# Kernel tuning notes

Measured on AMD Instinct MI355X. Metric: run time of the kernel, lower is better.

## Reference

```python
import jax, jax.numpy as jnp
import numpy as np

EPS = 1e-6

def _l2normalize(x, axis=1):
    # matches torch: x / sqrt(sum(x^2) + eps)
    norm = jnp.sqrt(jnp.sum(x * x, axis=axis, keepdims=True) + EPS)
    return x / norm


def setup_inputs() -> dict:
    key = jax.random.key(0)
    k1, k2, k3 = jax.random.split(key, 3)
    B, C, H, W = 8, 64, 48, 48
    x = jax.random.normal(k1, (B, C, H, W), dtype=jnp.float32)
    v = jax.random.normal(k2, (B, C, H, W), dtype=jnp.float32)
    pos = jax.random.normal(k3, (B, C, H, W), dtype=jnp.float32)
    # learned scalar parameters (init values from the torch module)
    gamma = jnp.float32(0.0)
    beta_gamma = jnp.float32(10.0)
    sum_gamma0 = jnp.float32(0.0)
    sum_gamma1 = jnp.float32(0.0)
    return {"x": x, "v": v, "pos": pos, "gamma": gamma,
            "beta_gamma": beta_gamma, "sum_gamma0": sum_gamma0,
            "sum_gamma1": sum_gamma1}


def reference(x, v, pos, gamma, beta_gamma, sum_gamma0, sum_gamma1):
    B, C, H, W = x.shape
    N = H * W
    # q and k are computed identically in the original module; compute once.
    q = _l2normalize(x + gamma * pos, axis=1)          # [B, C, H, W]
    qf = q.reshape(B, C, N)                             # [B, C, N]
    vf = v.reshape(B, v.shape[1], N)                    # [B, Cv, N]
    # scores[b, n, m] = <q[:, n], k[:, m]>; learned temperature beta_gamma
    scores = jnp.einsum('bcn,bcm->bnm', qf, qf) * beta_gamma  # [B, N, N]
    beta = jax.nn.softmax(scores, axis=-1)              # [B, N, N]
    # o = v @ beta^T  => o[b, c, n] = sum_m v[b, c, m] * beta[b, n, m]
    o = jnp.einsum('bcm,bnm->bcn', vf, beta).reshape(B, vf.shape[1], H, W)
    e0 = jnp.exp(sum_gamma0)
    e1 = jnp.exp(sum_gamma1)
    tot = e0 + e1
    out = (e0 / tot) * o + (e1 / tot) * v
    return out, beta.reshape(B, N, H, W)
```

## Files before the change

kernel.cpp:

```cpp
#include <hip/hip_runtime.h>
#include <hip/hip_bf16.h>

#define B_  8
#define C_  64
#define N_  2304
#define TS  64
#define NT_ (N_ / TS)
#define LDP 72

typedef __attribute__((ext_vector_type(8))) short  short8;
typedef __attribute__((ext_vector_type(4))) float  floatx4;

struct Hdr { int f32mode; float gamma, bg, cmax, w0, w1; };

__device__ __forceinline__ float bf2f(unsigned short u) {
  return __uint_as_float(((unsigned int)u) << 16);
}
__device__ __forceinline__ unsigned short f2bf(float f) {
  unsigned int x = __float_as_uint(f);
  x += 0x7fff + ((x >> 16) & 1);
  return (unsigned short)(x >> 16);
}

__global__ void detect_k(const void* g, const void* bgp, const void* s0,
                         const void* s1, Hdr* h) {
  if (threadIdx.x == 0 && blockIdx.x == 0) {
    int f32 = (((const unsigned short*)bgp)[0] == 0) ? 1 : 0;
    float gamma, bg, sg0, sg1;
    if (f32) {
      gamma = ((const float*)g)[0];  bg  = ((const float*)bgp)[0];
      sg0   = ((const float*)s0)[0]; sg1 = ((const float*)s1)[0];
    } else {
      gamma = bf2f(((const unsigned short*)g)[0]);
      bg    = bf2f(((const unsigned short*)bgp)[0]);
      sg0   = bf2f(((const unsigned short*)s0)[0]);
      sg1   = bf2f(((const unsigned short*)s1)[0]);
    }
    float e0 = __expf(sg0), e1 = __expf(sg1);
    h->f32mode = f32;
    h->gamma = gamma;
    h->bg = bg;
    h->cmax = fabsf(bg);
    h->w0 = e0 / (e0 + e1);
    h->w1 = e1 / (e0 + e1);
  }
}

__global__ __launch_bounds__(256)
void prep_q(const void* __restrict__ xv, const void* __restrict__ posv,
            const void* __restrict__ vv_raw, const Hdr* __restrict__ h,
            unsigned short* __restrict__ qT, unsigned short* __restrict__ vb) {
  int t = blockIdx.x * 256 + threadIdx.x;
  int b = t / N_;
  int n = t - b * N_;
  const bool f32 = h->f32mode;
  float gamma = h->gamma;
  float vals[C_];
  float s = 0.f;
  if (f32) {
    const float* xp = (const float*)xv  + (size_t)b * C_ * N_ + n;
    const float* pp = (const float*)posv + (size_t)b * C_ * N_ + n;
#pragma unroll
    for (int c = 0; c < C_; ++c) {
      float val = xp[(size_t)c * N_] + gamma * pp[(size_t)c * N_];
      vals[c] = val;  s += val * val;
    }
  } else {
    const unsigned short* xp = (const unsigned short*)xv  + (size_t)b * C_ * N_ + n;
    const unsigned short* pp = (const unsigned short*)posv + (size_t)b * C_ * N_ + n;
#pragma unroll
    for (int c = 0; c < C_; ++c) {
      float val = bf2f(xp[(size_t)c * N_]) + gamma * bf2f(pp[(size_t)c * N_]);
      vals[c] = val;  s += val * val;
    }
  }
  float inv = rsqrtf(s + 1e-6f);
  unsigned int* qrow = reinterpret_cast<unsigned int*>(qT + (size_t)t * C_);
#pragma unroll
  for (int c = 0; c < C_; c += 2) {
    qrow[c >> 1] = (unsigned int)f2bf(vals[c] * inv)
                 | ((unsigned int)f2bf(vals[c + 1] * inv) << 16);
  }
  const int NU32 = (B_ * C_ * N_) / 2;
  const int TC   = (B_ * N_);
  unsigned int* vb32 = reinterpret_cast<unsigned int*>(vb);
  if (f32) {
    const float* vf = (const float*)vv_raw;
    for (int i = t; i < NU32; i += TC) {
      float f0 = vf[2 * i], f1 = vf[2 * i + 1];
      vb32[i] = (unsigned int)f2bf(f0) | ((unsigned int)f2bf(f1) << 16);
    }
  } else {
    const unsigned int* v32 = (const unsigned int*)vv_raw;
    for (int i = t; i < NU32; i += TC) vb32[i] = v32[i];
  }
}

__global__ __launch_bounds__(256)
void pass1_rowsum(const unsigned short* __restrict__ qT,
                  const Hdr* __restrict__ h,
                  float* __restrict__ rowsum) {
  __shared__ unsigned short qm[TS * LDP];
  int b  = blockIdx.x / NT_;
  int n0 = (blockIdx.x - b * NT_) * TS;
  int tid  = threadIdx.x;
  int wave = tid >> 6;
  int lane = tid & 63;
  int quad = lane >> 4;
  int l15  = lane & 15;
  float bg = h->bg, cmax = h->cmax;
  const unsigned short* abase =
      qT + ((size_t)(b * N_ + n0 + 16 * wave + l15)) * C_ + quad * 8;
  short8 a0 = *reinterpret_cast<const short8*>(abase);
  short8 a1 = *reinterpret_cast<const short8*>(abase + 32);
  float acc[4] = {0.f, 0.f, 0.f, 0.f};
  for (int mt = 0; mt < NT_; ++mt) {
    int m0 = mt * TS;
    __syncthreads();
#pragma unroll
    for (int k = 0; k < 2; ++k) {
      int chunk = tid + 256 * k;
      int row = chunk >> 3;
      int col = (chunk & 7) * 8;
      short8 vv = *reinterpret_cast<const short8*>(
          qT + ((size_t)(b * N_ + m0 + row)) * C_ + col);
      *reinterpret_cast<short8*>(&qm[row * LDP + col]) = vv;
    }
    __syncthreads();
#pragma unroll
    for (int j = 0; j < 4; ++j) {
      short8 b0 = *reinterpret_cast<const short8*>(&qm[(j * 16 + l15) * LDP + quad * 8]);
      short8 b1 = *reinterpret_cast<const short8*>(&qm[(j * 16 + l15) * LDP + 32 + quad * 8]);
      floatx4 d = {0.f, 0.f, 0.f, 0.f};
      d = __builtin_amdgcn_mfma_f32_16x16x32_bf16(a0, b0, d, 0, 0, 0);
      d = __builtin_amdgcn_mfma_f32_16x16x32_bf16(a1, b1, d, 0, 0, 0);
#pragma unroll
      for (int r = 0; r < 4; ++r)
        acc[r] += __expf(d[r] * bg - cmax);
    }
  }
#pragma unroll
  for (int r = 0; r < 4; ++r) {
    float vv = acc[r];
    vv += __shfl_xor(vv, 1);
    vv += __shfl_xor(vv, 2);
    vv += __shfl_xor(vv, 4);
    vv += __shfl_xor(vv, 8);
    acc[r] = vv;
  }
  if (l15 == 0) {
#pragma unroll
    for (int r = 0; r < 4; ++r)
      rowsum[(size_t)b * N_ + n0 + 16 * wave + quad * 4 + r] = acc[r];
  }
}

__global__ __launch_bounds__(256)
void pass2_attn(const unsigned short* __restrict__ qT,
                const unsigned short* __restrict__ vb,
                const void* __restrict__ vraw,
                const Hdr* __restrict__ h,
                const float* __restrict__ rowsum,
                void* __restrict__ dout) {
  __shared__ unsigned short qm[TS * LDP];
  __shared__ unsigned short vt[TS * LDP];
  __shared__ unsigned short pt[TS * LDP];
  int b  = blockIdx.x / NT_;
  int n0 = (blockIdx.x - b * NT_) * TS;
  int tid  = threadIdx.x;
  int wave = tid >> 6;
  int lane = tid & 63;
  int quad = lane >> 4;
  int l15  = lane & 15;
  const bool f32 = h->f32mode;
  float bg = h->bg, cmax = h->cmax, w0 = h->w0, w1 = h->w1;
  unsigned short* out16  = (unsigned short*)dout;
  unsigned short* beta16 = out16 + (size_t)B_ * C_ * N_;
  float* out32  = (float*)dout;
  float* beta32 = out32 + (size_t)B_ * C_ * N_;

  const unsigned short* abase =
      qT + ((size_t)(b * N_ + n0 + 16 * wave + l15)) * C_ + quad * 8;
  short8 a0 = *reinterpret_cast<const short8*>(abase);
  short8 a1 = *reinterpret_cast<const short8*>(abase + 32);
  float inv[4];
#pragma unroll
  for (int r = 0; r < 4; ++r)
    inv[r] = 1.f / rowsum[(size_t)b * N_ + n0 + 16 * wave + quad * 4 + r];
  floatx4 oacc[4] = {{0.f,0.f,0.f,0.f},{0.f,0.f,0.f,0.f},
                     {0.f,0.f,0.f,0.f},{0.f,0.f,0.f,0.f}};
  for (int mt = 0; mt < NT_; ++mt) {
    int m0 = mt * TS;
    __syncthreads();
#pragma unroll
    for (int k = 0; k < 2; ++k) {
      int chunk = tid + 256 * k;
      int row = chunk >> 3;
      int col = (chunk & 7) * 8;
      short8 qv = *reinterpret_cast<const short8*>(
          qT + ((size_t)(b * N_ + m0 + row)) * C_ + col);
      *reinterpret_cast<short8*>(&qm[row * LDP + col]) = qv;
      short8 vv = *reinterpret_cast<const short8*>(
          vb + ((size_t)(b * C_ + row)) * N_ + m0 + col);
      *reinterpret_cast<short8*>(&vt[row * LDP + col]) = vv;
    }
    __syncthreads();
#pragma unroll
    for (int j = 0; j < 4; ++j) {
      short8 b0 = *reinterpret_cast<const short8*>(&qm[(j * 16 + l15) * LDP + quad * 8]);
      short8 b1 = *reinterpret_cast<const short8*>(&qm[(j * 16 + l15) * LDP + 32 + quad * 8]);
      floatx4 d = {0.f, 0.f, 0.f, 0.f};
      d = __builtin_amdgcn_mfma_f32_16x16x32_bf16(a0, b0, d, 0, 0, 0);
      d = __builtin_amdgcn_mfma_f32_16x16x32_bf16(a1, b1, d, 0, 0, 0);
#pragma unroll
      for (int r = 0; r < 4; ++r) {
        float p = __expf(d[r] * bg - cmax) * inv[r];
        pt[(16 * wave + quad * 4 + r) * LDP + j * 16 + l15] = f2bf(p);
        if (f32) {
          beta32[((size_t)(b * N_ + n0 + 16 * wave + quad * 4 + r)) * N_
                 + m0 + j * 16 + l15] = p;
        }
      }
    }
    __syncthreads();
    if (!f32) {
#pragma unroll
      for (int k = 0; k < 2; ++k) {
        int chunk = tid + 256 * k;
        int row = chunk >> 3;
        int col = (chunk & 7) * 8;
        short8 pv = *reinterpret_cast<const short8*>(&pt[row * LDP + col]);
        *reinterpret_cast<short8*>(
            beta16 + ((size_t)(b * N_ + n0 + row)) * N_ + m0 + col) = pv;
      }
    }
    short8 av0 = *reinterpret_cast<const short8*>(&vt[(16 * wave + l15) * LDP + quad * 8]);
    short8 av1 = *reinterpret_cast<const short8*>(&vt[(16 * wave + l15) * LDP + 32 + quad * 8]);
#pragma unroll
    for (int j = 0; j < 4; ++j) {
      short8 bp0 = *reinterpret_cast<const short8*>(&pt[(j * 16 + l15) * LDP + quad * 8]);
      short8 bp1 = *reinterpret_cast<const short8*>(&pt[(j * 16 + l15) * LDP + 32 + quad * 8]);
      oacc[j] = __builtin_amdgcn_mfma_f32_16x16x32_bf16(av0, bp0, oacc[j], 0, 0, 0);
      oacc[j] = __builtin_amdgcn_mfma_f32_16x16x32_bf16(av1, bp1, oacc[j], 0, 0, 0);
    }
  }
#pragma unroll
  for (int j = 0; j < 4; ++j) {
#pragma unroll
    for (int r = 0; r < 4; ++r) {
      int c = 16 * wave + quad * 4 + r;
      int n = n0 + 16 * j + l15;
      size_t idx = ((size_t)(b * C_ + c)) * N_ + n;
      if (f32) {
        float vvf = ((const float*)vraw)[idx];
        out32[idx] = w0 * oacc[j][r] + w1 * vvf;
      } else {
        float vvf = bf2f(((const unsigned short*)vraw)[idx]);
        out16[idx] = f2bf(w0 * oacc[j][r] + w1 * vvf);
      }
    }
  }
}

extern "C" void kernel_launch(void* const* d_in, const int* in_sizes, int n_in,
                              void* d_out, int out_size, void* d_ws, size_t ws_size,
                              hipStream_t stream) {
  const void* x     = d_in[0];
  const void* v     = d_in[1];
  const void* pos   = d_in[2];
  const void* gamma = d_in[3];
  const void* bg    = d_in[4];
  const void* sg0   = d_in[5];
  const void* sg1   = d_in[6];

  char* ws = (char*)d_ws;
  Hdr* hdr = (Hdr*)ws;
  unsigned short* qT = (unsigned short*)(ws + 256);
  unsigned short* vb = (unsigned short*)(ws + 256 + (size_t)B_ * N_ * C_ * 2);
  float* rowsum = (float*)(ws + 256 + (size_t)B_ * N_ * C_ * 4);

  detect_k<<<dim3(1), dim3(64), 0, stream>>>(gamma, bg, sg0, sg1, hdr);
  prep_q<<<dim3((B_ * N_) / 256), dim3(256), 0, stream>>>(x, pos, v, hdr, qT, vb);
  pass1_rowsum<<<dim3(B_ * NT_), dim3(256), 0, stream>>>(qT, hdr, rowsum);
  pass2_attn<<<dim3(B_ * NT_), dim3(256), 0, stream>>>(qT, vb, v, hdr, rowsum, d_out);
}
```

Measured before the change: 273.0 us.

## Split key dimension across four blocks and reduce partial sums in blend kernel

Both attention passes now split the key loop into four chunks, so the grid grows from 288 to 1152 blocks and fills the GPU's compute units. Pass 1 writes per-split partial row sums, which pass 2 adds together. Pass 2 writes fp32 partial outputs that a new blend kernel reduces and mixes with v. The bf16 conversion of v moves from prep_q into pass1, and prep_q uses 64-thread blocks. The cost is extra workspace traffic for four fp32 partial output copies plus one more kernel launch.

```diff
diff --git a/kernel.cpp b/kernel.cpp
--- a/kernel.cpp
+++ b/kernel.cpp
@@ -7,6 +7,8 @@
 #define TS  64
 #define NT_ (N_ / TS)
 #define LDP 72
+#define SPL 4
+#define MTS (NT_ / SPL)
 
 typedef __attribute__((ext_vector_type(8))) short  short8;
 typedef __attribute__((ext_vector_type(4))) float  floatx4;
@@ -46,11 +48,10 @@
   }
 }
 
-__global__ __launch_bounds__(256)
+__global__ __launch_bounds__(64)
 void prep_q(const void* __restrict__ xv, const void* __restrict__ posv,
-            const void* __restrict__ vv_raw, const Hdr* __restrict__ h,
-            unsigned short* __restrict__ qT, unsigned short* __restrict__ vb) {
-  int t = blockIdx.x * 256 + threadIdx.x;
+            const Hdr* __restrict__ h, unsigned short* __restrict__ qT) {
+  int t = blockIdx.x * 64 + threadIdx.x;
   int b = t / N_;
   int n = t - b * N_;
   const bool f32 = h->f32mode;
@@ -81,29 +82,41 @@
     qrow[c >> 1] = (unsigned int)f2bf(vals[c] * inv)
                  | ((unsigned int)f2bf(vals[c + 1] * inv) << 16);
   }
-  const int NU32 = (B_ * C_ * N_) / 2;
-  const int TC   = (B_ * N_);
-  unsigned int* vb32 = reinterpret_cast<unsigned int*>(vb);
-  if (f32) {
-    const float* vf = (const float*)vv_raw;
-    for (int i = t; i < NU32; i += TC) {
-      float f0 = vf[2 * i], f1 = vf[2 * i + 1];
-      vb32[i] = (unsigned int)f2bf(f0) | ((unsigned int)f2bf(f1) << 16);
-    }
-  } else {
-    const unsigned int* v32 = (const unsigned int*)vv_raw;
-    for (int i = t; i < NU32; i += TC) vb32[i] = v32[i];
-  }
 }
 
 __global__ __launch_bounds__(256)
 void pass1_rowsum(const unsigned short* __restrict__ qT,
+                  const void* __restrict__ vraw,
                   const Hdr* __restrict__ h,
-                  float* __restrict__ rowsum) {
+                  unsigned short* __restrict__ vb,
+                  float* __restrict__ rowsum_part) {
   __shared__ unsigned short qm[TS * LDP];
-  int b  = blockIdx.x / NT_;
-  int n0 = (blockIdx.x - b * NT_) * TS;
-  int tid  = threadIdx.x;
+  int bx  = blockIdx.x;
+  int tid = threadIdx.x;
+  {
+    int t = bx * 256 + tid;
+    unsigned int* vb32 = reinterpret_cast<unsigned int*>(vb);
+    if (h->f32mode) {
+      const float* vf = (const float*)vraw;
+#pragma unroll
+      for (int k = 0; k < 2; ++k) {
+        int i = t + k * 294912;
+        float f0 = vf[2 * i], f1 = vf[2 * i + 1];
+        vb32[i] = (unsigned int)f2bf(f0) | ((unsigned int)f2bf(f1) << 16);
+      }
+    } else {
+      const unsigned int* v32 = (const unsigned int*)vraw;
+#pragma unroll
+      for (int k = 0; k < 2; ++k) {
+        int i = t + k * 294912;
+        vb32[i] = v32[i];
+      }
+    }
+  }
+  int s  = bx & (SPL - 1);
+  int nt = (bx >> 2) % NT_;
+  int b  = bx / (SPL * NT_);
+  int n0 = nt * TS;
   int wave = tid >> 6;
   int lane = tid & 63;
   int quad = lane >> 4;
@@ -114,7 +127,8 @@
   short8 a0 = *reinterpret_cast<const short8*>(abase);
   short8 a1 = *reinterpret_cast<const short8*>(abase + 32);
   float acc[4] = {0.f, 0.f, 0.f, 0.f};
-  for (int mt = 0; mt < NT_; ++mt) {
+  int mt0 = s * MTS;
+  for (int mt = mt0; mt < mt0 + MTS; ++mt) {
     int m0 = mt * TS;
     __syncthreads();
 #pragma unroll
@@ -151,33 +165,36 @@
   if (l15 == 0) {
 #pragma unroll
     for (int r = 0; r < 4; ++r)
-      rowsum[(size_t)b * N_ + n0 + 16 * wave + quad * 4 + r] = acc[r];
+      rowsum_part[((size_t)(b * N_ + n0 + 16 * wave + quad * 4 + r)) * SPL + s]
+          = acc[r];
   }
 }
 
 __global__ __launch_bounds__(256)
 void pass2_attn(const unsigned short* __restrict__ qT,
                 const unsigned short* __restrict__ vb,
-                const void* __restrict__ vraw,
                 const Hdr* __restrict__ h,
-                const float* __restrict__ rowsum,
+                const float* __restrict__ rowsum_part,
+                float* __restrict__ opart,
                 void* __restrict__ dout) {
   __shared__ unsigned short qm[TS * LDP];
   __shared__ unsigned short vt[TS * LDP];
   __shared__ unsigned short pt[TS * LDP];
-  int b  = blockIdx.x / NT_;
-  int n0 = (blockIdx.x - b * NT_) * TS;
+  int bx = blockIdx.x;
+  int s  = bx & (SPL - 1);
+  int nt = (bx >> 2) % NT_;
+  int b  = bx / (SPL * NT_);
+  int n0 = nt * TS;
   int tid  = threadIdx.x;
   int wave = tid >> 6;
   int lane = tid & 63;
   int quad = lane >> 4;
   int l15  = lane & 15;
   const bool f32 = h->f32mode;
-  float bg = h->bg, cmax = h->cmax, w0 = h->w0, w1 = h->w1;
+  float bg = h->bg, cmax = h->cmax;
   unsigned short* out16  = (unsigned short*)dout;
   unsigned short* beta16 = out16 + (size_t)B_ * C_ * N_;
-  float* out32  = (float*)dout;
-  float* beta32 = out32 + (size_t)B_ * C_ * N_;
+  float* beta32 = (float*)dout + (size_t)B_ * C_ * N_;
 
   const unsigned short* abase =
       qT + ((size_t)(b * N_ + n0 + 16 * wave + l15)) * C_ + quad * 8;
@@ -185,11 +202,15 @@
   short8 a1 = *reinterpret_cast<const short8*>(abase + 32);
   float inv[4];
 #pragma unroll
-  for (int r = 0; r < 4; ++r)
-    inv[r] = 1.f / rowsum[(size_t)b * N_ + n0 + 16 * wave + quad * 4 + r];
+  for (int r = 0; r < 4; ++r) {
+    floatx4 rs = *reinterpret_cast<const floatx4*>(
+        rowsum_part + ((size_t)(b * N_ + n0 + 16 * wave + quad * 4 + r)) * SPL);
+    inv[r] = 1.f / (rs[0] + rs[1] + rs[2] + rs[3]);
+  }
   floatx4 oacc[4] = {{0.f,0.f,0.f,0.f},{0.f,0.f,0.f,0.f},
                      {0.f,0.f,0.f,0.f},{0.f,0.f,0.f,0.f}};
-  for (int mt = 0; mt < NT_; ++mt) {
+  int mtb = s * MTS;
+  for (int mt = mtb; mt < mtb + MTS; ++mt) {
     int m0 = mt * TS;
     __syncthreads();
 #pragma unroll
@@ -244,21 +265,47 @@
       oacc[j] = __builtin_amdgcn_mfma_f32_16x16x32_bf16(av1, bp1, oacc[j], 0, 0, 0);
     }
   }
+  float* op = opart + (size_t)s * (B_ * C_ * N_);
 #pragma unroll
   for (int j = 0; j < 4; ++j) {
 #pragma unroll
     for (int r = 0; r < 4; ++r) {
       int c = 16 * wave + quad * 4 + r;
       int n = n0 + 16 * j + l15;
-      size_t idx = ((size_t)(b * C_ + c)) * N_ + n;
-      if (f32) {
-        float vvf = ((const float*)vraw)[idx];
-        out32[idx] = w0 * oacc[j][r] + w1 * vvf;
-      } else {
-        float vvf = bf2f(((const unsigned short*)vraw)[idx]);
-        out16[idx] = f2bf(w0 * oacc[j][r] + w1 * vvf);
-      }
-    }
+      op[((size_t)(b * C_ + c)) * N_ + n] = oacc[j][r];
+    }
+  }
+}
+
+__global__ __launch_bounds__(256)
+void blend_k(const float* __restrict__ opart, const void* __restrict__ vraw,
+             const Hdr* __restrict__ h, void* __restrict__ dout) {
+  int t = blockIdx.x * 256 + threadIdx.x;
+  const int STR = (B_ * C_ * N_) / 4;
+  const floatx4* p = reinterpret_cast<const floatx4*>(opart);
+  floatx4 o  = p[t];
+  floatx4 o1 = p[t + STR];
+  floatx4 o2 = p[t + 2 * STR];
+  floatx4 o3 = p[t + 3 * STR];
+#pragma unroll
+  for (int k = 0; k < 4; ++k) o[k] = (o[k] + o1[k]) + (o2[k] + o3[k]);
+  float w0 = h->w0, w1 = h->w1;
+  if (h->f32mode) {
+    floatx4 vv = reinterpret_cast<const floatx4*>(vraw)[t];
+    floatx4 r;
+#pragma unroll
+    for (int k = 0; k < 4; ++k) r[k] = w0 * o[k] + w1 * vv[k];
+    reinterpret_cast<floatx4*>(dout)[t] = r;
+  } else {
+    unsigned long long v64 =
+        reinterpret_cast<const unsigned long long*>(vraw)[t];
+    unsigned long long rr = 0;
+#pragma unroll
+    for (int k = 0; k < 4; ++k) {
+      float vf = bf2f((unsigned short)(v64 >> (16 * k)));
+      rr |= ((unsigned long long)f2bf(w0 * o[k] + w1 * vf)) << (16 * k);
+    }
+    reinterpret_cast<unsigned long long*>(dout)[t] = rr;
   }
 }
 
@@ -276,11 +323,13 @@
   char* ws = (char*)d_ws;
   Hdr* hdr = (Hdr*)ws;
   unsigned short* qT = (unsigned short*)(ws + 256);
-  unsigned short* vb = (unsigned short*)(ws + 256 + (size_t)B_ * N_ * C_ * 2);
-  float* rowsum = (float*)(ws + 256 + (size_t)B_ * N_ * C_ * 4);
+  unsigned short* vb = qT + (size_t)B_ * N_ * C_;
+  float* rowsum_part = (float*)(ws + 256 + (size_t)B_ * N_ * C_ * 4);
+  float* opart = rowsum_part + (size_t)B_ * N_ * SPL;
 
   detect_k<<<dim3(1), dim3(64), 0, stream>>>(gamma, bg, sg0, sg1, hdr);
-  prep_q<<<dim3((B_ * N_) / 256), dim3(256), 0, stream>>>(x, pos, v, hdr, qT, vb);
-  pass1_rowsum<<<dim3(B_ * NT_), dim3(256), 0, stream>>>(qT, hdr, rowsum);
-  pass2_attn<<<dim3(B_ * NT_), dim3(256), 0, stream>>>(qT, vb, v, hdr, rowsum, d_out);
-}
+  prep_q<<<dim3((B_ * N_) / 64), dim3(64), 0, stream>>>(x, pos, hdr, qT);
+  pass1_rowsum<<<dim3(B_ * NT_ * SPL), dim3(256), 0, stream>>>(qT, v, hdr, vb, rowsum_part);
+  pass2_attn<<<dim3(B_ * NT_ * SPL), dim3(256), 0, stream>>>(qT, vb, hdr, rowsum_part, opart, d_out);
+  blend_k<<<dim3((B_ * C_ * N_) / 1024), dim3(256), 0, stream>>>(opart, v, hdr, d_out);
+}
```

Result: faster. 225.1 us (-17.6%).
